# Performance work log

Hardware: AMD Instinct MI355X
Metric: run time of the kernel (lower is better)

Reference implementation:

```python
import jax, jax.numpy as jnp
import numpy as np

N = 50000      # nodes
E = 800000     # edges (before self loops)
IN_DIM = 128
HID = 16
HEADS = 8
OUT_DIM = 40
NEG_SLOPE = 0.2


def setup_inputs() -> dict:
    key = jax.random.key(0)
    ks = jax.random.split(key, 10)
    x = jax.random.normal(ks[0], (N, IN_DIM), jnp.float32)
    edge_index = jax.random.randint(ks[1], (2, E), 0, N, dtype=jnp.int32)
    # layer 1: GATConv(IN_DIM, HID, heads=HEADS, concat=True)
    W1 = jax.random.normal(ks[2], (IN_DIM, HEADS * HID), jnp.float32) / np.sqrt(IN_DIM).astype(np.float32)
    att_src1 = jax.random.normal(ks[3], (HEADS, HID), jnp.float32) * 0.1
    att_dst1 = jax.random.normal(ks[4], (HEADS, HID), jnp.float32) * 0.1
    bias1 = jnp.zeros((HEADS * HID,), jnp.float32)
    # layer 2: GATConv(HEADS*HID, OUT_DIM, heads=1, concat=False)
    W2 = jax.random.normal(ks[5], (HEADS * HID, OUT_DIM), jnp.float32) / np.sqrt(HEADS * HID).astype(np.float32)
    att_src2 = jax.random.normal(ks[6], (1, OUT_DIM), jnp.float32) * 0.1
    att_dst2 = jax.random.normal(ks[7], (1, OUT_DIM), jnp.float32) * 0.1
    bias2 = jnp.zeros((OUT_DIM,), jnp.float32)
    return {"x": x, "W1": W1, "att_src1": att_src1, "att_dst1": att_dst1, "bias1": bias1,
            "W2": W2, "att_src2": att_src2, "att_dst2": att_dst2, "bias2": bias2,
            "edge_index": edge_index}


def gat_conv(x, src, dst, W, att_src, att_dst, bias, heads, dim, concat, num_nodes):
    # h: [N, H, D]
    h = (x @ W).reshape(num_nodes, heads, dim)
    a_src = jnp.sum(h * att_src, axis=-1)  # [N, H]
    a_dst = jnp.sum(h * att_dst, axis=-1)  # [N, H]
    e = a_src[src] + a_dst[dst]            # [E', H]
    e = jnp.where(e > 0, e, NEG_SLOPE * e)  # leaky_relu
    # segment softmax over edges sharing the same target node
    m = jax.ops.segment_max(e, dst, num_segments=num_nodes)  # [N, H]
    e = jnp.exp(e - m[dst])
    s = jax.ops.segment_sum(e, dst, num_segments=num_nodes)  # [N, H]
    alpha = e / (s[dst] + 1e-16)            # [E', H]
    msg = h[src] * alpha[:, :, None]        # [E', H, D]
    out = jax.ops.segment_sum(msg, dst, num_segments=num_nodes)  # [N, H, D]
    if concat:
        out = out.reshape(num_nodes, heads * dim)
    else:
        out = out.mean(axis=1)
    return out + bias


def reference(x, W1, att_src1, att_dst1, bias1, W2, att_src2, att_dst2, bias2, edge_index):
    # add self loops (PyG GATConv default)
    loop = jnp.arange(N, dtype=edge_index.dtype)
    src = jnp.concatenate([edge_index[0], loop])
    dst = jnp.concatenate([edge_index[1], loop])
    # eval mode: dropout (p=0.6) is identity
    h = gat_conv(x, src, dst, W1, att_src1, att_dst1, bias1, HEADS, HID, True, N)
    h = jax.nn.elu(h)
    out = gat_conv(h, src, dst, W2, att_src2, att_dst2, bias2, 1, OUT_DIM, False, N)
    return jax.nn.log_softmax(out, axis=1)
```

## Files before the change

### kernel.cpp

```cpp
#include <hip/hip_runtime.h>
#include <math.h>

#define IN_DIM 128
#define HEADS 8
#define HID 16
#define OUT_DIM 40
#define NEG 0.2f
#define NSLICE 8
#define PREP_BLOCKS 96

typedef short bf16x8 __attribute__((ext_vector_type(8)));
typedef float f32x4 __attribute__((ext_vector_type(4)));

__device__ __forceinline__ unsigned short f32_to_bf16_rne(float v) {
  unsigned u = __float_as_uint(v);
  return (unsigned short)((u + 0x7FFFu + ((u >> 16) & 1u)) >> 16);
}

__global__ void prep_hist_k(const float* __restrict__ W1, const float* __restrict__ as1,
                            const float* __restrict__ ad1, const float* __restrict__ W2,
                            const float* __restrict__ as2, const float* __restrict__ ad2,
                            unsigned short* __restrict__ whi, unsigned short* __restrict__ wlo,
                            unsigned short* __restrict__ w2p,
                            const int* __restrict__ ei, int E0, int N, int snode,
                            int* __restrict__ deg) {
  if ((int)blockIdx.x >= PREP_BLOCKS) {
    int b = blockIdx.x - PREP_BLOCKS;
    int slice = b & (NSLICE - 1);
    int e = (b >> 3) * 256 + threadIdx.x;
    int EP = E0 + N;
    if (e >= EP) return;
    int d = (e < E0) ? ei[E0 + e] : (e - E0);
    if (d / snode == slice) atomicAdd(&deg[d], 1);
    return;
  }
  int t = blockIdx.x * 256 + threadIdx.x;
  if (t < 18432) {
    int j = t & 7, lane = (t >> 3) & 63, kc = (t >> 9) & 3, ct = t >> 11;
    int k = kc * 32 + (lane >> 4) * 8 + j;
    int col = lane & 15;
    float v;
    if (ct < 8) {
      v = W1[k * 128 + ct * 16 + col];
    } else {
      int h = col & 7;
      const float* att = (col < 8) ? as1 : ad1;
      float s = 0.f;
      #pragma unroll
      for (int d = 0; d < 16; ++d) s += W1[k * 128 + h * 16 + d] * att[h * 16 + d];
      v = s;
    }
    unsigned u = __float_as_uint(v);
    unsigned hi = (u + 0x7FFFu + ((u >> 16) & 1u)) >> 16;
    float rem = v - __uint_as_float(hi << 16);
    unsigned ur = __float_as_uint(rem);
    unsigned lo = (ur + 0x7FFFu + ((ur >> 16) & 1u)) >> 16;
    whi[t] = (unsigned short)hi;
    wlo[t] = (unsigned short)lo;
  } else if (t < 18432 + 6144) {
    int u2 = t - 18432;
    int j = u2 & 7, lane = (u2 >> 3) & 63, kc = (u2 >> 9) & 3, ct = u2 >> 11;
    int k = kc * 32 + (lane >> 4) * 8 + j;
    int col = ct * 16 + (lane & 15);
    float v;
    if (col < OUT_DIM) {
      v = W2[k * OUT_DIM + col];
    } else if (col < 42) {
      const float* att = (col == OUT_DIM) ? as2 : ad2;
      float s = 0.f;
      #pragma unroll 8
      for (int d = 0; d < OUT_DIM; ++d) s += W2[k * OUT_DIM + d] * att[d];
      v = s;
    } else {
      v = 0.f;
    }
    w2p[u2] = f32_to_bf16_rne(v);
  }
}

__global__ __launch_bounds__(1024) void scanA_k(const int* __restrict__ deg, int* __restrict__ rp,
                                                int* __restrict__ bsum, int n) {
  __shared__ int wsum[16];
  int tid = threadIdx.x;
  int i = blockIdx.x * 1024 + tid;
  int lane = tid & 63, w = tid >> 6;
  int v = (i < n) ? deg[i] : 0;
  int x = v;
  #pragma unroll
  for (int off = 1; off < 64; off <<= 1) {
    int y = __shfl_up(x, off);
    if (lane >= off) x += y;
  }
  if (lane == 63) wsum[w] = x;
  __syncthreads();
  if (tid < 16) {
    int s = wsum[tid];
    #pragma unroll
    for (int off = 1; off < 16; off <<= 1) {
      int y = __shfl_up(s, off);
      if (tid >= off) s += y;
    }
    wsum[tid] = s;
  }
  __syncthreads();
  int woff = (w == 0) ? 0 : wsum[w - 1];
  if (i < n) rp[i] = woff + x - v;
  if (tid == 0) bsum[blockIdx.x] = wsum[15];
}

__global__ __launch_bounds__(1024) void scanBC_k(const int* __restrict__ bsum, int nb,
                                                 int* __restrict__ rp, int* __restrict__ cnt, int n) {
  __shared__ int wsum[16];
  __shared__ int offs[1025];
  int tid = threadIdx.x;
  int lane = tid & 63, w = tid >> 6;
  int v = (tid < nb) ? bsum[tid] : 0;
  int x = v;
  #pragma unroll
  for (int off = 1; off < 64; off <<= 1) {
    int y = __shfl_up(x, off);
    if (lane >= off) x += y;
  }
  if (lane == 63) wsum[w] = x;
  __syncthreads();
  if (tid < 16) {
    int s = wsum[tid];
    #pragma unroll
    for (int off = 1; off < 16; off <<= 1) {
      int y = __shfl_up(s, off);
      if (tid >= off) s += y;
    }
    wsum[tid] = s;
  }
  __syncthreads();
  int woff = (w == 0) ? 0 : wsum[w - 1];
  if (tid < nb) offs[tid + 1] = woff + x;
  if (tid == 0) offs[0] = 0;
  __syncthreads();
  int add = offs[blockIdx.x];
  int i = blockIdx.x * 1024 + tid;
  if (i < n) {
    int val = rp[i] + add;
    rp[i] = val;
    cnt[i] = val;
  }
  if (blockIdx.x == 0 && tid == 0) rp[n] = offs[nb];
}

__global__ __launch_bounds__(256) void gemm1_scatter_k(
    const float* __restrict__ x, const unsigned short* __restrict__ whi,
    const unsigned short* __restrict__ wlo,
    unsigned short* __restrict__ h1, float* __restrict__ a1s, float* __restrict__ a1d,
    int N, int G1,
    const int* __restrict__ ei, int E0, int snode,
    int* __restrict__ cnt, int* __restrict__ csr_src) {
  if ((int)blockIdx.x >= G1) {
    int b = blockIdx.x - G1;
    int slice = b & (NSLICE - 1);
    int e = (b >> 3) * 256 + threadIdx.x;
    int EP = E0 + N;
    if (e >= EP) return;
    int d = (e < E0) ? ei[E0 + e] : (e - E0);
    if (d / snode != slice) return;
    int s = (e < E0) ? ei[e] : d;
    int pos = atomicAdd(&cnt[d], 1);
    csr_src[pos] = s;
    return;
  }
  int w = threadIdx.x >> 6, lane = threadIdx.x & 63;
  int quad = lane >> 4, l15 = lane & 15;
  int row = blockIdx.x * 64 + w * 16 + l15;
  int rowc = (row < N) ? row : (N - 1);

  f32x4 acc[9];
  #pragma unroll
  for (int t = 0; t < 9; ++t) acc[t] = (f32x4){0.f, 0.f, 0.f, 0.f};

  const float* xr = x + (size_t)rowc * 128 + quad * 8;
  #pragma unroll
  for (int kc = 0; kc < 4; ++kc) {
    f32x4 a0 = *reinterpret_cast<const f32x4*>(xr + kc * 32);
    f32x4 a1 = *reinterpret_cast<const f32x4*>(xr + kc * 32 + 4);
    float av[8] = {a0.x, a0.y, a0.z, a0.w, a1.x, a1.y, a1.z, a1.w};
    bf16x8 ahi, alo;
    #pragma unroll
    for (int j = 0; j < 8; ++j) {
      unsigned u = __float_as_uint(av[j]);
      unsigned hi = (u + 0x7FFFu + ((u >> 16) & 1u)) >> 16;
      float rem = av[j] - __uint_as_float(hi << 16);
      unsigned ur = __float_as_uint(rem);
      unsigned lo = (ur + 0x7FFFu + ((ur >> 16) & 1u)) >> 16;
      ahi[j] = (short)hi;
      alo[j] = (short)lo;
    }
    #pragma unroll
    for (int ct = 0; ct < 9; ++ct) {
      bf16x8 bh = *reinterpret_cast<const bf16x8*>(whi + ((size_t)(ct * 4 + kc) * 64 + lane) * 8);
      bf16x8 bl = *reinterpret_cast<const bf16x8*>(wlo + ((size_t)(ct * 4 + kc) * 64 + lane) * 8);
      acc[ct] = __builtin_amdgcn_mfma_f32_16x16x32_bf16(ahi, bh, acc[ct], 0, 0, 0);
      acc[ct] = __builtin_amdgcn_mfma_f32_16x16x32_bf16(ahi, bl, acc[ct], 0, 0, 0);
      acc[ct] = __builtin_amdgcn_mfma_f32_16x16x32_bf16(alo, bh, acc[ct], 0, 0, 0);
    }
  }
  int rbase = blockIdx.x * 64 + w * 16 + quad * 4;
  #pragma unroll
  for (int reg = 0; reg < 4; ++reg) {
    int r = rbase + reg;
    if (r < N) {
      #pragma unroll
      for (int ct = 0; ct < 8; ++ct)
        h1[(size_t)r * 128 + ct * 16 + l15] = f32_to_bf16_rne(acc[ct][reg]);
      float v = acc[8][reg];
      if (l15 < 8) a1s[r * 8 + l15] = v;
      else         a1d[r * 8 + (l15 - 8)] = v;
    }
  }
}

__global__ __launch_bounds__(256) void agg1_k(
    const int* __restrict__ row_ptr, const int* __restrict__ csr_src,
    const float* __restrict__ a1s, const float* __restrict__ a1d,
    const unsigned* __restrict__ h1u, const float* __restrict__ bias1,
    unsigned* __restrict__ vrowp, int N) {
  int wid = threadIdx.x >> 6;
  int lane = threadIdx.x & 63;
  int n = blockIdx.x * 4 + wid;

  __shared__ __align__(16) float wls_s[4][8 * 132];
  __shared__ __align__(16) int   srcs_s[4][128];

  if (n >= N) return;
  float* wls  = wls_s[wid];
  int*   srcs = srcs_s[wid];

  int rs = row_ptr[n], re = row_ptr[n + 1];
  int deg = re - rs;
  int h = lane >> 3;

  float accx = 0.f, accy = 0.f, inv;

  if (deg <= 128) {
    for (int i0 = lane; i0 < deg; i0 += 64) srcs[i0] = csr_src[rs + i0];
    int slot = lane >> 3, hw = lane & 7;
    float adn = a1d[n * 8 + hw];
    float sw = 0.f;
    for (int i0 = 0; i0 < deg; i0 += 16) {
      int ia = i0 + slot, ib = i0 + 8 + slot;
      bool va = ia < deg, vb = ib < deg;
      int sa = srcs[va ? ia : 0];
      int sb = srcs[vb ? ib : 0];
      float ea = a1s[sa * 8 + hw] + adn;
      float eb = a1s[sb * 8 + hw] + adn;
      ea = fmaxf(ea, NEG * ea);
      eb = fmaxf(eb, NEG * eb);
      float wa = va ? __expf(ea) : 0.f;
      float wb = vb ? __expf(eb) : 0.f;
      sw += wa + wb;
      if (va) wls[hw * 132 + ia] = wa;
      if (vb) wls[hw * 132 + ib] = wb;
    }
    sw += __shfl_xor(sw, 8);
    sw += __shfl_xor(sw, 16);
    sw += __shfl_xor(sw, 32);
    inv = __shfl(1.f / (sw + 1e-16f), h);

    const float* wh = wls + h * 132;
    int i = 0;
    for (; i + 16 <= deg; i += 16) {
      int4 sa = *reinterpret_cast<const int4*>(srcs + i);
      int4 sb = *reinterpret_cast<const int4*>(srcs + i + 4);
      int4 sc = *reinterpret_cast<const int4*>(srcs + i + 8);
      int4 sd = *reinterpret_cast<const int4*>(srcs + i + 12);
      float4 wa = *reinterpret_cast<const float4*>(wh + i);
      float4 wb = *reinterpret_cast<const float4*>(wh + i + 4);
      float4 wc = *reinterpret_cast<const float4*>(wh + i + 8);
      float4 wd = *reinterpret_cast<const float4*>(wh + i + 12);
      unsigned u0 = h1u[(size_t)sa.x * 64 + lane];
      unsigned u1 = h1u[(size_t)sa.y * 64 + lane];
      unsigned u2 = h1u[(size_t)sa.z * 64 + lane];
      unsigned u3 = h1u[(size_t)sa.w * 64 + lane];
      unsigned u4 = h1u[(size_t)sb.x * 64 + lane];
      unsigned u5 = h1u[(size_t)sb.y * 64 + lane];
      unsigned u6 = h1u[(size_t)sb.z * 64 + lane];
      unsigned u7 = h1u[(size_t)sb.w * 64 + lane];
      unsigned u8 = h1u[(size_t)sc.x * 64 + lane];
      unsigned u9 = h1u[(size_t)sc.y * 64 + lane];
      unsigned uA = h1u[(size_t)sc.z * 64 + lane];
      unsigned uB = h1u[(size_t)sc.w * 64 + lane];
      unsigned uC = h1u[(size_t)sd.x * 64 + lane];
      unsigned uD = h1u[(size_t)sd.y * 64 + lane];
      unsigned uE = h1u[(size_t)sd.z * 64 + lane];
      unsigned uF = h1u[(size_t)sd.w * 64 + lane];
      accx += wa.x * __uint_as_float(u0 << 16) + wa.y * __uint_as_float(u1 << 16)
            + wa.z * __uint_as_float(u2 << 16) + wa.w * __uint_as_float(u3 << 16)
            + wb.x * __uint_as_float(u4 << 16) + wb.y * __uint_as_float(u5 << 16)
            + wb.z * __uint_as_float(u6 << 16) + wb.w * __uint_as_float(u7 << 16)
            + wc.x * __uint_as_float(u8 << 16) + wc.y * __uint_as_float(u9 << 16)
            + wc.z * __uint_as_float(uA << 16) + wc.w * __uint_as_float(uB << 16)
            + wd.x * __uint_as_float(uC << 16) + wd.y * __uint_as_float(uD << 16)
            + wd.z * __uint_as_float(uE << 16) + wd.w * __uint_as_float(uF << 16);
      accy += wa.x * __uint_as_float(u0 & 0xFFFF0000u) + wa.y * __uint_as_float(u1 & 0xFFFF0000u)
            + wa.z * __uint_as_float(u2 & 0xFFFF0000u) + wa.w * __uint_as_float(u3 & 0xFFFF0000u)
            + wb.x * __uint_as_float(u4 & 0xFFFF0000u) + wb.y * __uint_as_float(u5 & 0xFFFF0000u)
            + wb.z * __uint_as_float(u6 & 0xFFFF0000u) + wb.w * __uint_as_float(u7 & 0xFFFF0000u)
            + wc.x * __uint_as_float(u8 & 0xFFFF0000u) + wc.y * __uint_as_float(u9 & 0xFFFF0000u)
            + wc.z * __uint_as_float(uA & 0xFFFF0000u) + wc.w * __uint_as_float(uB & 0xFFFF0000u)
            + wd.x * __uint_as_float(uC & 0xFFFF0000u) + wd.y * __uint_as_float(uD & 0xFFFF0000u)
            + wd.z * __uint_as_float(uE & 0xFFFF0000u) + wd.w * __uint_as_float(uF & 0xFFFF0000u);
    }
    for (; i + 4 <= deg; i += 4) {
      int4 sa = *reinterpret_cast<const int4*>(srcs + i);
      float4 wa = *reinterpret_cast<const float4*>(wh + i);
      unsigned u0 = h1u[(size_t)sa.x * 64 + lane];
      unsigned u1 = h1u[(size_t)sa.y * 64 + lane];
      unsigned u2 = h1u[(size_t)sa.z * 64 + lane];
      unsigned u3 = h1u[(size_t)sa.w * 64 + lane];
      accx += wa.x * __uint_as_float(u0 << 16) + wa.y * __uint_as_float(u1 << 16)
            + wa.z * __uint_as_float(u2 << 16) + wa.w * __uint_as_float(u3 << 16);
      accy += wa.x * __uint_as_float(u0 & 0xFFFF0000u) + wa.y * __uint_as_float(u1 & 0xFFFF0000u)
            + wa.z * __uint_as_float(u2 & 0xFFFF0000u) + wa.w * __uint_as_float(u3 & 0xFFFF0000u);
    }
    for (; i < deg; ++i) {
      int s = srcs[i];
      float w = wh[i];
      unsigned u = h1u[(size_t)s * 64 + lane];
      accx += w * __uint_as_float(u << 16);
      accy += w * __uint_as_float(u & 0xFFFF0000u);
    }
  } else {
    float adn = a1d[n * 8 + h];
    float sw = 0.f;
    for (int i = rs; i < re; ++i) {
      int s = csr_src[i];
      float e = a1s[s * 8 + h] + adn;
      e = fmaxf(e, NEG * e);
      float w = __expf(e);
      unsigned u = h1u[(size_t)s * 64 + lane];
      sw += w;
      accx += w * __uint_as_float(u << 16);
      accy += w * __uint_as_float(u & 0xFFFF0000u);
    }
    inv = 1.f / (sw + 1e-16f);
  }

  float2 b = *reinterpret_cast<const float2*>(bias1 + 2 * lane);
  float vx = accx * inv + b.x;
  float vy = accy * inv + b.y;
  vx = (vx > 0.f) ? vx : (__expf(vx) - 1.f);
  vy = (vy > 0.f) ? vy : (__expf(vy) - 1.f);
  unsigned packed = (unsigned)f32_to_bf16_rne(vx) | ((unsigned)f32_to_bf16_rne(vy) << 16);
  vrowp[(size_t)n * 64 + lane] = packed;
}

__global__ __launch_bounds__(256) void gemm2_mfma_k(
    const unsigned short* __restrict__ vrow, const unsigned short* __restrict__ w2p,
    unsigned short* __restrict__ h2, float* __restrict__ a2s, float* __restrict__ a2d, int N) {
  int w = threadIdx.x >> 6, lane = threadIdx.x & 63;
  int quad = lane >> 4, l15 = lane & 15;
  int row = blockIdx.x * 64 + w * 16 + l15;
  int rowc = (row < N) ? row : (N - 1);

  f32x4 acc[3];
  #pragma unroll
  for (int t = 0; t < 3; ++t) acc[t] = (f32x4){0.f, 0.f, 0.f, 0.f};

  const unsigned short* vr = vrow + (size_t)rowc * 128 + quad * 8;
  #pragma unroll
  for (int kc = 0; kc < 4; ++kc) {
    bf16x8 a = *reinterpret_cast<const bf16x8*>(vr + kc * 32);
    #pragma unroll
    for (int ct = 0; ct < 3; ++ct) {
      bf16x8 bfrag = *reinterpret_cast<const bf16x8*>(w2p + ((size_t)(ct * 4 + kc) * 64 + lane) * 8);
      acc[ct] = __builtin_amdgcn_mfma_f32_16x16x32_bf16(a, bfrag, acc[ct], 0, 0, 0);
    }
  }
  int rbase = blockIdx.x * 64 + w * 16 + quad * 4;
  #pragma unroll
  for (int reg = 0; reg < 4; ++reg) {
    int r = rbase + reg;
    if (r < N) {
      #pragma unroll
      for (int ct = 0; ct < 3; ++ct) {
        int col = ct * 16 + l15;
        float v = acc[ct][reg];
        if (col < OUT_DIM)       h2[(size_t)r * 64 + col] = f32_to_bf16_rne(v);
        else if (col == OUT_DIM) a2s[r] = v;
        else if (col == 41)      a2d[r] = v;
      }
    }
  }
}

__global__ __launch_bounds__(256) void agg2_k(
    const int* __restrict__ row_ptr, const int* __restrict__ csr_src,
    const float* __restrict__ a2s, const float* __restrict__ a2d,
    const unsigned* __restrict__ h2u, const float* __restrict__ bias2,
    float* __restrict__ out, int N) {
  int wid = threadIdx.x >> 6;
  int lane = threadIdx.x & 63;
  int n = blockIdx.x * 4 + wid;

  __shared__ __align__(16) float wls_s[4][128];
  __shared__ __align__(16) int   srcs_s[4][128];

  if (n >= N) return;
  float* wls  = wls_s[wid];
  int*   srcs = srcs_s[wid];

  int rs = row_ptr[n], re = row_ptr[n + 1];
  int deg = re - rs;
  float adn = a2d[n];
  int pair = lane >> 5;
  int c32  = lane & 31;
  float accx = 0.f, accy = 0.f, inv;

  if (deg <= 128) {
    for (int i0 = lane; i0 < deg; i0 += 64) srcs[i0] = csr_src[rs + i0];
    int ia = lane, ib = lane + 64;
    bool va = ia < deg, vb = ib < deg;
    int sa = srcs[va ? ia : 0];
    int sb = srcs[vb ? ib : 0];
    float ea = a2s[sa] + adn;
    float eb = a2s[sb] + adn;
    ea = fmaxf(ea, NEG * ea);
    eb = fmaxf(eb, NEG * eb);
    float wa = va ? __expf(ea) : 0.f;
    float wb = vb ? __expf(eb) : 0.f;
    float sw = wa + wb;
    if (va) wls[ia] = wa;
    if (vb) wls[ib] = wb;
    #pragma unroll
    for (int off = 32; off > 0; off >>= 1) sw += __shfl_xor(sw, off);
    inv = 1.f / (sw + 1e-16f);

    int i = 0;
    for (; i + 16 <= deg; i += 16) {
      #pragma unroll
      for (int j = 0; j < 8; ++j) {
        int idx = i + 2 * j + pair;
        int s = srcs[idx];
        float w = wls[idx];
        unsigned g = h2u[(size_t)s * 32 + c32];
        accx += w * __uint_as_float(g << 16);
        accy += w * __uint_as_float(g & 0xFFFF0000u);
      }
    }
    for (; i < deg; i += 2) {
      int idx = i + pair;
      bool val = idx < deg;
      int s = srcs[val ? idx : 0];
      float w = val ? wls[idx] : 0.f;
      unsigned g = h2u[(size_t)s * 32 + c32];
      accx += w * __uint_as_float(g << 16);
      accy += w * __uint_as_float(g & 0xFFFF0000u);
    }
  } else {
    float sw = 0.f;
    for (int i = rs; i < re; i += 2) {
      int idx = i + pair;
      bool val = idx < re;
      int s = csr_src[val ? idx : rs];
      float e = a2s[s] + adn;
      e = fmaxf(e, NEG * e);
      float w = val ? __expf(e) : 0.f;
      sw += w;
      unsigned g = h2u[(size_t)s * 32 + c32];
      accx += w * __uint_as_float(g << 16);
      accy += w * __uint_as_float(g & 0xFFFF0000u);
    }
    #pragma unroll
    for (int off = 32; off > 0; off >>= 1) sw += __shfl_xor(sw, off);
    inv = 32.f / (sw + 1e-16f);
  }

  accx += __shfl_xor(accx, 32);
  accy += __shfl_xor(accy, 32);
  int c0 = 2 * c32, c1 = 2 * c32 + 1;
  bool a0 = (lane < 32) && (c0 < OUT_DIM);
  bool a1 = (lane < 32) && (c1 < OUT_DIM);
  float v0 = a0 ? (accx * inv + bias2[c0]) : -1e30f;
  float v1 = a1 ? (accy * inv + bias2[c1]) : -1e30f;
  float vm = fmaxf(v0, v1);
  #pragma unroll
  for (int off = 32; off > 0; off >>= 1) vm = fmaxf(vm, __shfl_xor(vm, off));
  float ex = (a0 ? __expf(v0 - vm) : 0.f) + (a1 ? __expf(v1 - vm) : 0.f);
  #pragma unroll
  for (int off = 32; off > 0; off >>= 1) ex += __shfl_xor(ex, off);
  if (lane < OUT_DIM / 2) {
    float le = __logf(ex);
    float2 o = make_float2(v0 - vm - le, v1 - vm - le);
    *reinterpret_cast<float2*>(out + (size_t)n * OUT_DIM + c0) = o;
  }
}


extern "C" void kernel_launch(void* const* d_in, const int* in_sizes, int n_in,
                              void* d_out, int out_size, void* d_ws, size_t ws_size,
                              hipStream_t stream) {
  const float* x   = (const float*)d_in[0];
  const float* W1  = (const float*)d_in[1];
  const float* as1 = (const float*)d_in[2];
  const float* ad1 = (const float*)d_in[3];
  const float* b1  = (const float*)d_in[4];
  const float* W2  = (const float*)d_in[5];
  const float* as2 = (const float*)d_in[6];
  const float* ad2 = (const float*)d_in[7];
  const float* b2  = (const float*)d_in[8];
  const int*   ei  = (const int*)d_in[9];
  int N  = in_sizes[0] / IN_DIM;
  int E0 = in_sizes[9] / 2;
  int EP = E0 + N;
  int snode = (N + NSLICE - 1) / NSLICE;
  float* out = (float*)d_out;

  char* ws = (char*)d_ws;
  size_t off = 0;
  auto alloc = [&](size_t bytes) {
    char* p = ws + off;
    off += (bytes + 255) & ~size_t(255);
    return p;
  };
  unsigned short* h1   = (unsigned short*)alloc((size_t)N * 128 * 2);
  float* a1s  = (float*)alloc((size_t)N * 8 * 4);
  float* a1d  = (float*)alloc((size_t)N * 8 * 4);
  unsigned*       vrow = (unsigned*)alloc((size_t)N * 64 * 4);
  unsigned short* h2   = (unsigned short*)alloc((size_t)N * 64 * 2);
  float* a2s  = (float*)alloc((size_t)N * 4);
  float* a2d  = (float*)alloc((size_t)N * 4);
  int*   deg  = (int*)alloc((size_t)N * 4);
  int*   cnt  = (int*)alloc((size_t)N * 4);
  int*   rp   = (int*)alloc((size_t)(N + 4) * 4);
  int*   bsum = (int*)alloc((size_t)1024 * 4);
  int*   csr  = (int*)alloc((size_t)EP * 4);
  unsigned short* whi = (unsigned short*)alloc((size_t)18432 * 2);
  unsigned short* wlo = (unsigned short*)alloc((size_t)18432 * 2);
  unsigned short* w2p = (unsigned short*)alloc((size_t)6144 * 2);

  int nb = (N + 1023) / 1024;
  int nchunk = (EP + 255) / 256;
  int G1 = (N + 63) / 64;

  hipMemsetAsync(deg, 0, (size_t)N * 4, stream);
  prep_hist_k<<<PREP_BLOCKS + nchunk * NSLICE, 256, 0, stream>>>(
      W1, as1, ad1, W2, as2, ad2, whi, wlo, w2p, ei, E0, N, snode, deg);
  scanA_k<<<nb, 1024, 0, stream>>>(deg, rp, bsum, N);
  scanBC_k<<<nb, 1024, 0, stream>>>(bsum, nb, rp, cnt, N);
  gemm1_scatter_k<<<G1 + nchunk * NSLICE, 256, 0, stream>>>(
      x, whi, wlo, h1, a1s, a1d, N, G1, ei, E0, snode, cnt, csr);
  agg1_k<<<(N + 3) / 4, 256, 0, stream>>>(rp, csr, a1s, a1d, (const unsigned*)h1, b1, vrow, N);
  gemm2_mfma_k<<<G1, 256, 0, stream>>>((const unsigned short*)vrow, w2p, h2, a2s, a2d, N);
  agg2_k<<<(N + 3) / 4, 256, 0, stream>>>(rp, csr, a2s, a2d, (const unsigned*)h2, b2, out, N);
}
```

Measured before the change: 263.8 us.

## Fuse CSR build into persistent kernel with software grid barriers

Merges weight prep, degree histogram, two-level scan, and CSR scatter into one persistent 256-block kernel that separates phases with atomic-counter grid barriers. This replaces several kernel launches. The CSR scatter no longer shares a launch with the layer-1 GEMM, so the two stop overlapping and now run back to back. It relies on all 256 blocks being co-resident and adds spin-wait barrier overhead. Each block also loops over many more edge chunks than before, which reduces parallelism in the histogram and scatter phases.

```diff
diff --git a/kernel.cpp b/kernel.cpp
--- a/kernel.cpp
+++ b/kernel.cpp
@@ -6,8 +6,7 @@
 #define HID 16
 #define OUT_DIM 40
 #define NEG 0.2f
-#define NSLICE 8
-#define PREP_BLOCKS 96
+#define NBLK 256
 
 typedef short bf16x8 __attribute__((ext_vector_type(8)));
 typedef float f32x4 __attribute__((ext_vector_type(4)));
@@ -17,156 +16,177 @@
   return (unsigned short)((u + 0x7FFFu + ((u >> 16) & 1u)) >> 16);
 }
 
-__global__ void prep_hist_k(const float* __restrict__ W1, const float* __restrict__ as1,
-                            const float* __restrict__ ad1, const float* __restrict__ W2,
-                            const float* __restrict__ as2, const float* __restrict__ ad2,
-                            unsigned short* __restrict__ whi, unsigned short* __restrict__ wlo,
-                            unsigned short* __restrict__ w2p,
-                            const int* __restrict__ ei, int E0, int N, int snode,
-                            int* __restrict__ deg) {
-  if ((int)blockIdx.x >= PREP_BLOCKS) {
-    int b = blockIdx.x - PREP_BLOCKS;
-    int slice = b & (NSLICE - 1);
-    int e = (b >> 3) * 256 + threadIdx.x;
-    int EP = E0 + N;
-    if (e >= EP) return;
-    int d = (e < E0) ? ei[E0 + e] : (e - E0);
-    if (d / snode == slice) atomicAdd(&deg[d], 1);
-    return;
-  }
-  int t = blockIdx.x * 256 + threadIdx.x;
-  if (t < 18432) {
-    int j = t & 7, lane = (t >> 3) & 63, kc = (t >> 9) & 3, ct = t >> 11;
-    int k = kc * 32 + (lane >> 4) * 8 + j;
-    int col = lane & 15;
-    float v;
-    if (ct < 8) {
-      v = W1[k * 128 + ct * 16 + col];
-    } else {
-      int h = col & 7;
-      const float* att = (col < 8) ? as1 : ad1;
-      float s = 0.f;
+__device__ __forceinline__ void grid_bar(int* bar, int phase) {
+  __syncthreads();
+  if (threadIdx.x == 0) {
+    __threadfence();
+    __hip_atomic_fetch_add(bar, 1, __ATOMIC_RELEASE, __HIP_MEMORY_SCOPE_AGENT);
+    int target = (int)gridDim.x * phase;
+    while (__hip_atomic_load(bar, __ATOMIC_ACQUIRE, __HIP_MEMORY_SCOPE_AGENT) < target)
+      __builtin_amdgcn_s_sleep(2);
+    __threadfence();
+  }
+  __syncthreads();
+}
+
+__global__ __launch_bounds__(256, 2) void csr_k(
+    const float* __restrict__ W1, const float* __restrict__ as1, const float* __restrict__ ad1,
+    const float* __restrict__ W2, const float* __restrict__ as2, const float* __restrict__ ad2,
+    unsigned short* __restrict__ whi, unsigned short* __restrict__ wlo,
+    unsigned short* __restrict__ w2p,
+    const int* __restrict__ ei, int E0, int N, int snode,
+    int* __restrict__ deg, int* __restrict__ rp, int* __restrict__ bsum,
+    int* __restrict__ cnt, int* __restrict__ csr, int* __restrict__ bar) {
+  const int tid = threadIdx.x;
+  const int b = blockIdx.x;
+  const int EP = E0 + N;
+  __shared__ int wsum[5];
+
+  {
+    int t = b * 256 + tid;
+    if (t < 18432) {
+      int j = t & 7, lane = (t >> 3) & 63, kc = (t >> 9) & 3, ct = t >> 11;
+      int k = kc * 32 + (lane >> 4) * 8 + j;
+      int col = lane & 15;
+      float v;
+      if (ct < 8) {
+        v = W1[k * 128 + ct * 16 + col];
+      } else {
+        int h = col & 7;
+        const float* att = (col < 8) ? as1 : ad1;
+        float s = 0.f;
+        #pragma unroll
+        for (int d = 0; d < 16; ++d) s += W1[k * 128 + h * 16 + d] * att[h * 16 + d];
+        v = s;
+      }
+      unsigned u = __float_as_uint(v);
+      unsigned hi = (u + 0x7FFFu + ((u >> 16) & 1u)) >> 16;
+      float rem = v - __uint_as_float(hi << 16);
+      unsigned ur = __float_as_uint(rem);
+      unsigned lo = (ur + 0x7FFFu + ((ur >> 16) & 1u)) >> 16;
+      whi[t] = (unsigned short)hi;
+      wlo[t] = (unsigned short)lo;
+    } else if (t < 18432 + 6144) {
+      int u2 = t - 18432;
+      int j = u2 & 7, lane = (u2 >> 3) & 63, kc = (u2 >> 9) & 3, ct = u2 >> 11;
+      int k = kc * 32 + (lane >> 4) * 8 + j;
+      int col = ct * 16 + (lane & 15);
+      float v;
+      if (col < OUT_DIM) {
+        v = W2[k * OUT_DIM + col];
+      } else if (col < 42) {
+        const float* att = (col == OUT_DIM) ? as2 : ad2;
+        float s = 0.f;
+        #pragma unroll 8
+        for (int d = 0; d < OUT_DIM; ++d) s += W2[k * OUT_DIM + d] * att[d];
+        v = s;
+      } else {
+        v = 0.f;
+      }
+      w2p[u2] = f32_to_bf16_rne(v);
+    }
+  }
+  grid_bar(bar, 1);
+
+  {
+    int slice = b & 7;
+    int nchE = (EP + 255) >> 8;
+    for (int c = (b >> 3); c < nchE; c += (NBLK >> 3)) {
+      int e = (c << 8) + tid;
+      if (e < EP) {
+        int d = (e < E0) ? ei[E0 + e] : (e - E0);
+        if (d / snode == slice) atomicAdd(&deg[d], 1);
+      }
+    }
+  }
+  grid_bar(bar, 2);
+
+  {
+    int nc2 = (N + 255) >> 8;
+    for (int c = b; c < nc2; c += NBLK) {
+      int i = (c << 8) + tid;
+      int v = (i < N) ? deg[i] : 0;
+      int lane = tid & 63, w = tid >> 6;
+      int x = v;
       #pragma unroll
-      for (int d = 0; d < 16; ++d) s += W1[k * 128 + h * 16 + d] * att[h * 16 + d];
-      v = s;
-    }
-    unsigned u = __float_as_uint(v);
-    unsigned hi = (u + 0x7FFFu + ((u >> 16) & 1u)) >> 16;
-    float rem = v - __uint_as_float(hi << 16);
-    unsigned ur = __float_as_uint(rem);
-    unsigned lo = (ur + 0x7FFFu + ((ur >> 16) & 1u)) >> 16;
-    whi[t] = (unsigned short)hi;
-    wlo[t] = (unsigned short)lo;
-  } else if (t < 18432 + 6144) {
-    int u2 = t - 18432;
-    int j = u2 & 7, lane = (u2 >> 3) & 63, kc = (u2 >> 9) & 3, ct = u2 >> 11;
-    int k = kc * 32 + (lane >> 4) * 8 + j;
-    int col = ct * 16 + (lane & 15);
-    float v;
-    if (col < OUT_DIM) {
-      v = W2[k * OUT_DIM + col];
-    } else if (col < 42) {
-      const float* att = (col == OUT_DIM) ? as2 : ad2;
-      float s = 0.f;
-      #pragma unroll 8
-      for (int d = 0; d < OUT_DIM; ++d) s += W2[k * OUT_DIM + d] * att[d];
-      v = s;
-    } else {
-      v = 0.f;
-    }
-    w2p[u2] = f32_to_bf16_rne(v);
-  }
-}
-
-__global__ __launch_bounds__(1024) void scanA_k(const int* __restrict__ deg, int* __restrict__ rp,
-                                                int* __restrict__ bsum, int n) {
-  __shared__ int wsum[16];
-  int tid = threadIdx.x;
-  int i = blockIdx.x * 1024 + tid;
-  int lane = tid & 63, w = tid >> 6;
-  int v = (i < n) ? deg[i] : 0;
-  int x = v;
-  #pragma unroll
-  for (int off = 1; off < 64; off <<= 1) {
-    int y = __shfl_up(x, off);
-    if (lane >= off) x += y;
-  }
-  if (lane == 63) wsum[w] = x;
-  __syncthreads();
-  if (tid < 16) {
-    int s = wsum[tid];
+      for (int off = 1; off < 64; off <<= 1) {
+        int y = __shfl_up(x, off);
+        if (lane >= off) x += y;
+      }
+      if (lane == 63) wsum[w] = x;
+      __syncthreads();
+      if (tid == 0) {
+        int a = 0;
+        #pragma unroll
+        for (int j = 0; j < 4; ++j) { int t2 = wsum[j]; wsum[j] = a; a += t2; }
+        wsum[4] = a;
+      }
+      __syncthreads();
+      int incl = wsum[w] + x;
+      if (i < N) rp[i] = incl - v;
+      if (tid == 0) bsum[c] = wsum[4];
+      __syncthreads();
+    }
+  }
+  grid_bar(bar, 3);
+
+  if (b == 0) {
+    int nc2 = (N + 255) >> 8;
+    int v = (tid < nc2) ? bsum[tid] : 0;
+    int lane = tid & 63, w = tid >> 6;
+    int x = v;
     #pragma unroll
-    for (int off = 1; off < 16; off <<= 1) {
-      int y = __shfl_up(s, off);
-      if (tid >= off) s += y;
-    }
-    wsum[tid] = s;
-  }
-  __syncthreads();
-  int woff = (w == 0) ? 0 : wsum[w - 1];
-  if (i < n) rp[i] = woff + x - v;
-  if (tid == 0) bsum[blockIdx.x] = wsum[15];
-}
-
-__global__ __launch_bounds__(1024) void scanBC_k(const int* __restrict__ bsum, int nb,
-                                                 int* __restrict__ rp, int* __restrict__ cnt, int n) {
-  __shared__ int wsum[16];
-  __shared__ int offs[1025];
-  int tid = threadIdx.x;
-  int lane = tid & 63, w = tid >> 6;
-  int v = (tid < nb) ? bsum[tid] : 0;
-  int x = v;
-  #pragma unroll
-  for (int off = 1; off < 64; off <<= 1) {
-    int y = __shfl_up(x, off);
-    if (lane >= off) x += y;
-  }
-  if (lane == 63) wsum[w] = x;
-  __syncthreads();
-  if (tid < 16) {
-    int s = wsum[tid];
-    #pragma unroll
-    for (int off = 1; off < 16; off <<= 1) {
-      int y = __shfl_up(s, off);
-      if (tid >= off) s += y;
-    }
-    wsum[tid] = s;
-  }
-  __syncthreads();
-  int woff = (w == 0) ? 0 : wsum[w - 1];
-  if (tid < nb) offs[tid + 1] = woff + x;
-  if (tid == 0) offs[0] = 0;
-  __syncthreads();
-  int add = offs[blockIdx.x];
-  int i = blockIdx.x * 1024 + tid;
-  if (i < n) {
-    int val = rp[i] + add;
-    rp[i] = val;
-    cnt[i] = val;
-  }
-  if (blockIdx.x == 0 && tid == 0) rp[n] = offs[nb];
-}
-
-__global__ __launch_bounds__(256) void gemm1_scatter_k(
+    for (int off = 1; off < 64; off <<= 1) {
+      int y = __shfl_up(x, off);
+      if (lane >= off) x += y;
+    }
+    if (lane == 63) wsum[w] = x;
+    __syncthreads();
+    if (tid == 0) {
+      int a = 0;
+      #pragma unroll
+      for (int j = 0; j < 4; ++j) { int t2 = wsum[j]; wsum[j] = a; a += t2; }
+      wsum[4] = a;
+    }
+    __syncthreads();
+    int incl = wsum[w] + x;
+    if (tid < nc2) bsum[tid] = incl;
+    if (tid == 0) rp[N] = wsum[4];
+  }
+  grid_bar(bar, 4);
+
+  {
+    for (int i = b * 256 + tid; i < N; i += NBLK * 256) {
+      int c = i >> 8;
+      int add = (c > 0) ? bsum[c - 1] : 0;
+      int val = rp[i] + add;
+      rp[i] = val;
+      cnt[i] = val;
+    }
+  }
+  grid_bar(bar, 5);
+
+  {
+    int slice = b & 7;
+    int nchE = (EP + 255) >> 8;
+    for (int c = (b >> 3); c < nchE; c += (NBLK >> 3)) {
+      int e = (c << 8) + tid;
+      if (e < EP) {
+        int d = (e < E0) ? ei[E0 + e] : (e - E0);
+        if (d / snode == slice) {
+          int s = (e < E0) ? ei[e] : d;
+          int pos = atomicAdd(&cnt[d], 1);
+          csr[pos] = s;
+        }
+      }
+    }
+  }
+}
+
+__global__ __launch_bounds__(256) void gemm1_mfma_k(
     const float* __restrict__ x, const unsigned short* __restrict__ whi,
     const unsigned short* __restrict__ wlo,
-    unsigned short* __restrict__ h1, float* __restrict__ a1s, float* __restrict__ a1d,
-    int N, int G1,
-    const int* __restrict__ ei, int E0, int snode,
-    int* __restrict__ cnt, int* __restrict__ csr_src) {
-  if ((int)blockIdx.x >= G1) {
-    int b = blockIdx.x - G1;
-    int slice = b & (NSLICE - 1);
-    int e = (b >> 3) * 256 + threadIdx.x;
-    int EP = E0 + N;
-    if (e >= EP) return;
-    int d = (e < E0) ? ei[E0 + e] : (e - E0);
-    if (d / snode != slice) return;
-    int s = (e < E0) ? ei[e] : d;
-    int pos = atomicAdd(&cnt[d], 1);
-    csr_src[pos] = s;
-    return;
-  }
+    unsigned short* __restrict__ h1, float* __restrict__ a1s, float* __restrict__ a1d, int N) {
   int w = threadIdx.x >> 6, lane = threadIdx.x & 63;
   int quad = lane >> 4, l15 = lane & 15;
   int row = blockIdx.x * 64 + w * 16 + l15;
@@ -510,7 +530,7 @@
   int N  = in_sizes[0] / IN_DIM;
   int E0 = in_sizes[9] / 2;
   int EP = E0 + N;
-  int snode = (N + NSLICE - 1) / NSLICE;
+  int snode = (N + 7) / 8;
   float* out = (float*)d_out;
 
   char* ws = (char*)d_ws;
@@ -527,7 +547,7 @@
   unsigned short* h2   = (unsigned short*)alloc((size_t)N * 64 * 2);
   float* a2s  = (float*)alloc((size_t)N * 4);
   float* a2d  = (float*)alloc((size_t)N * 4);
-  int*   deg  = (int*)alloc((size_t)N * 4);
+  int*   degbar = (int*)alloc(((size_t)N + 64) * 4);
   int*   cnt  = (int*)alloc((size_t)N * 4);
   int*   rp   = (int*)alloc((size_t)(N + 4) * 4);
   int*   bsum = (int*)alloc((size_t)1024 * 4);
@@ -535,18 +555,15 @@
   unsigned short* whi = (unsigned short*)alloc((size_t)18432 * 2);
   unsigned short* wlo = (unsigned short*)alloc((size_t)18432 * 2);
   unsigned short* w2p = (unsigned short*)alloc((size_t)6144 * 2);
-
-  int nb = (N + 1023) / 1024;
-  int nchunk = (EP + 255) / 256;
+  int* deg = degbar;
+  int* bar = degbar + N;
+
   int G1 = (N + 63) / 64;
 
-  hipMemsetAsync(deg, 0, (size_t)N * 4, stream);
-  prep_hist_k<<<PREP_BLOCKS + nchunk * NSLICE, 256, 0, stream>>>(
-      W1, as1, ad1, W2, as2, ad2, whi, wlo, w2p, ei, E0, N, snode, deg);
-  scanA_k<<<nb, 1024, 0, stream>>>(deg, rp, bsum, N);
-  scanBC_k<<<nb, 1024, 0, stream>>>(bsum, nb, rp, cnt, N);
-  gemm1_scatter_k<<<G1 + nchunk * NSLICE, 256, 0, stream>>>(
-      x, whi, wlo, h1, a1s, a1d, N, G1, ei, E0, snode, cnt, csr);
+  hipMemsetAsync(degbar, 0, ((size_t)N + 64) * 4, stream);
+  csr_k<<<NBLK, 256, 0, stream>>>(W1, as1, ad1, W2, as2, ad2, whi, wlo, w2p,
+                                  ei, E0, N, snode, deg, rp, bsum, cnt, csr, bar);
+  gemm1_mfma_k<<<G1, 256, 0, stream>>>(x, whi, wlo, h1, a1s, a1d, N);
   agg1_k<<<(N + 3) / 4, 256, 0, stream>>>(rp, csr, a1s, a1d, (const unsigned*)h1, b1, vrow, N);
   gemm2_mfma_k<<<G1, 256, 0, stream>>>((const unsigned short*)vrow, w2p, h2, a2s, a2d, N);
   agg2_k<<<(N + 3) / 4, 256, 0, stream>>>(rp, csr, a2s, a2d, (const unsigned*)h2, b2, out, N);
```

After: 417.3 us. 58.2% more time.
